# Kernel optimization log

Hardware: AMD Instinct MI355X
Metric: run time of the kernel (lower is better)

The kernel has to match this reference:

```python
import jax, jax.numpy as jnp
import numpy as np


def _banded_diag_mean(a, b, r):
    """For each (batch i, row j) return mean of (a[i] @ b[i].T)[j, j-r:j+r+1],
    computed without materializing the LxL matrix. Windows are clipped to
    [max(0,j-r), min(L, j+r+1)].  a, b: [B, L, D]."""
    B, L, _ = a.shape
    sums = jnp.zeros((B, L), a.dtype)
    counts = jnp.zeros((L,), a.dtype)
    for d in range(-r, r + 1):  # small fixed set of 2r+1 diagonals
        if d >= 0:
            dots = jnp.einsum('bld,bld->bl', a[:, :L - d], b[:, d:])
            sums = sums.at[:, :L - d].add(dots)
            counts = counts.at[:L - d].add(1.0)
        else:
            dots = jnp.einsum('bld,bld->bl', a[:, -d:], b[:, :L + d])
            sums = sums.at[:, -d:].add(dots)
            counts = counts.at[-d:].add(1.0)
    return sums / counts


def setup_inputs() -> dict:
    key = jax.random.key(0)
    k1, k2, k3 = jax.random.split(key, 3)
    B, L, D_in, D_feat = 8, 1024, 512, 256
    return {
        'feature1': jax.random.normal(k1, (B, L, D_in), jnp.float32),
        'feature2': jax.random.normal(k2, (B, L, D_in), jnp.float32),
        'W': jax.random.normal(k3, (D_in, D_feat), jnp.float32) / np.sqrt(D_in),
        'b': jnp.zeros((D_feat,), jnp.float32),
        'positive_range_self': 4,
        'positive_range_tgt': 4,
    }


def reference(feature1, feature2, W, b, positive_range_self, positive_range_tgt):
    # MLPLayer projection (shared eval_func for both inputs): linear + relu
    emb_1 = jax.nn.relu(feature1 @ W + b)  # [B, L, Df]
    emb_2 = jax.nn.relu(feature2 @ W + b)  # [B, L, Df]
    B, L, Df = emb_1.shape
    N = B * L

    positive = jnp.einsum('bld,bld->bl', emb_1, emb_2)  # [B, L]
    if positive_range_self > 0:
        positive = positive + _banded_diag_mean(emb_1, emb_1, positive_range_self)
        positive = positive + _banded_diag_mean(emb_2, emb_2, positive_range_self)
    if positive_range_tgt > 0:
        positive = positive + _banded_diag_mean(emb_1, emb_2, positive_range_tgt)
    positive = positive.reshape(N)

    e1 = emb_1.reshape(N, Df)
    e2 = emb_2.reshape(N, Df)
    sim_matrix = e1 @ e2.T  # [N, N]
    negative = jax.nn.logsumexp(sim_matrix, axis=-1) - jnp.log(jnp.asarray(N, sim_matrix.dtype))

    nce_loss = jnp.mean(-positive + negative)
    return nce_loss
```

## Files before the change

### kernel.cpp

```cpp
#include <hip/hip_runtime.h>
#include <hip/hip_bf16.h>
#include <math.h>

#define DIN 512
#define DF 256
#define LSEQ 1024
#define NTOT 8192

typedef __attribute__((ext_vector_type(8))) short short8;
typedef __attribute__((ext_vector_type(4))) short short4v;
typedef __attribute__((ext_vector_type(4))) float f32x4;

__device__ __forceinline__ short f2bf(float x) {
  union { float f; unsigned u; } un; un.f = x;
  unsigned r = un.u + 0x7fffu + ((un.u >> 16) & 1u);
  return (short)(r >> 16);
}
__device__ __forceinline__ float bf2f(short s) {
  union { unsigned u; float f; } un; un.u = ((unsigned)(unsigned short)s) << 16;
  return un.f;
}

typedef __attribute__((address_space(1))) const unsigned char AS1c;
typedef __attribute__((address_space(3))) unsigned char AS3;
__device__ __forceinline__ void gload16(const void* g, void* l) {
  __builtin_amdgcn_global_load_lds((AS1c*)g, (AS3*)l, 16, 0, 0);
}
#define CFENCE() asm volatile("" ::: "memory")

__global__ __launch_bounds__(256) void prep_w_kernel(const float* __restrict__ W,
                                                     short* __restrict__ Wt) {
  int idx = blockIdx.x * 256 + threadIdx.x;
  int c = idx >> 9;
  int k = idx & (DIN - 1);
  Wt[idx] = f2bf(W[(size_t)k * DF + c]);
}

#define PBM 64
#define PBK 64
#define PROW 72

__global__ __launch_bounds__(256) void proj_kernel(const float* __restrict__ f1,
                                                   const float* __restrict__ f2,
                                                   const short* __restrict__ Wt,
                                                   const float* __restrict__ bias,
                                                   short* __restrict__ emb1,
                                                   short* __restrict__ emb2) {
  const float* feat = blockIdx.y ? f2 : f1;
  short* emb = blockIdx.y ? emb2 : emb1;
  __shared__ short ldsA[PBM * PROW];
  __shared__ short ldsB[DF * PROW];
  const int tid = threadIdx.x;
  const int lane = tid & 63, wv = tid >> 6;
  const int wrow = (wv & 1) * 32, wcol = (wv >> 1) * 128;
  const int l15 = lane & 15, lk = (lane >> 4) * 8;
  const int rowbase = blockIdx.x * PBM;

  f32x4 acc[2][8];
#pragma unroll
  for (int mi = 0; mi < 2; ++mi)
#pragma unroll
    for (int nf = 0; nf < 8; ++nf) acc[mi][nf] = f32x4{0.f, 0.f, 0.f, 0.f};

  for (int kb = 0; kb < DIN; kb += PBK) {
    __syncthreads();
#pragma unroll
    for (int i = 0; i < 4; ++i) {
      int flat = tid * 4 + i;
      int r = flat >> 4, kq = (flat & 15) * 4;
      f32x4 v = *(const f32x4*)(feat + (size_t)(rowbase + r) * DIN + kb + kq);
      short4v h;
      h[0] = f2bf(v[0]); h[1] = f2bf(v[1]); h[2] = f2bf(v[2]); h[3] = f2bf(v[3]);
      *(short4v*)(ldsA + r * PROW + kq) = h;
    }
#pragma unroll
    for (int i = 0; i < 8; ++i) {
      int c = tid, kq = i * 8;
      short8 v = *(const short8*)(Wt + (size_t)c * DIN + kb + kq);
      *(short8*)(ldsB + c * PROW + kq) = v;
    }
    __syncthreads();
#pragma unroll
    for (int kk = 0; kk < 2; ++kk) {
      short8 af[2], bf[8];
#pragma unroll
      for (int mi = 0; mi < 2; ++mi)
        af[mi] = *(const short8*)(ldsA + (wrow + mi * 16 + l15) * PROW + kk * 32 + lk);
#pragma unroll
      for (int nf = 0; nf < 8; ++nf)
        bf[nf] = *(const short8*)(ldsB + (wcol + nf * 16 + l15) * PROW + kk * 32 + lk);
#pragma unroll
      for (int mi = 0; mi < 2; ++mi)
#pragma unroll
        for (int nf = 0; nf < 8; ++nf)
          acc[mi][nf] = __builtin_amdgcn_mfma_f32_16x16x32_bf16(af[mi], bf[nf], acc[mi][nf], 0, 0, 0);
    }
  }
  const int r4 = (lane >> 4) * 4;
#pragma unroll
  for (int mi = 0; mi < 2; ++mi) {
    int row0 = rowbase + wrow + mi * 16 + r4;
#pragma unroll
    for (int nf = 0; nf < 8; ++nf) {
      int col = wcol + nf * 16 + l15;
      float bb = bias[col];
#pragma unroll
      for (int r = 0; r < 4; ++r) {
        float v = acc[mi][nf][r] + bb;
        v = v > 0.f ? v : 0.f;
        emb[(size_t)(row0 + r) * DF + col] = f2bf(v);
      }
    }
  }
}

__global__ __launch_bounds__(64) void positive_kernel(const short* __restrict__ emb1,
                                                      const short* __restrict__ emb2,
                                                      const int* __restrict__ prs,
                                                      const int* __restrict__ prt,
                                                      float* __restrict__ pos) {
  const int row = blockIdx.x;
  const int b = row >> 10, j = row & (LSEQ - 1);
  const int lane = threadIdx.x;
  const int rs = prs[0], rt = prt[0];
  float a1[4], a2[4];
  {
    short4v v1 = *(const short4v*)(emb1 + (size_t)row * DF + lane * 4);
    short4v v2 = *(const short4v*)(emb2 + (size_t)row * DF + lane * 4);
#pragma unroll
    for (int i = 0; i < 4; ++i) { a1[i] = bf2f(v1[i]); a2[i] = bf2f(v2[i]); }
  }
  float dot12 = 0.f, p11 = 0.f, p22 = 0.f, p12 = 0.f;
#pragma unroll
  for (int i = 0; i < 4; ++i) dot12 += a1[i] * a2[i];
  int rmax = rs > rt ? rs : rt;
  for (int d = -rmax; d <= rmax; ++d) {
    int k = j + d;
    if (k < 0 || k >= LSEQ) continue;
    size_t koff = (size_t)(b * LSEQ + k) * DF + lane * 4;
    short4v w1 = *(const short4v*)(emb1 + koff);
    short4v w2 = *(const short4v*)(emb2 + koff);
    float d11 = 0.f, d22 = 0.f, d12 = 0.f;
#pragma unroll
    for (int i = 0; i < 4; ++i) {
      float e1k = bf2f(w1[i]), e2k = bf2f(w2[i]);
      d11 += a1[i] * e1k;
      d22 += a2[i] * e2k;
      d12 += a1[i] * e2k;
    }
    if (d >= -rs && d <= rs) { p11 += d11; p22 += d22; }
    if (d >= -rt && d <= rt) { p12 += d12; }
  }
#pragma unroll
  for (int m = 1; m < 64; m <<= 1) {
    dot12 += __shfl_xor(dot12, m);
    p11 += __shfl_xor(p11, m);
    p22 += __shfl_xor(p22, m);
    p12 += __shfl_xor(p12, m);
  }
  if (lane == 0) {
    float res = dot12;
    if (rs > 0) {
      int lo = j - rs < 0 ? 0 : j - rs;
      int hi = j + rs > LSEQ - 1 ? LSEQ - 1 : j + rs;
      res += (p11 + p22) / (float)(hi - lo + 1);
    }
    if (rt > 0) {
      int lo = j - rt < 0 ? 0 : j - rt;
      int hi = j + rt > LSEQ - 1 ? LSEQ - 1 : j + rt;
      res += p12 / (float)(hi - lo + 1);
    }
    pos[row] = res;
  }
}

#define NBM 128
#define NBN 32
#define NCHUNK 16
#define CHW (NTOT / NCHUNK)
#define NT (CHW / NBN)

__global__ __launch_bounds__(256, 3) void negative_kernel(const short* __restrict__ e1,
                                                          const short* __restrict__ e2,
                                                          float* __restrict__ mpart,
                                                          float* __restrict__ spart) {
  __shared__ short ldsB[2][NBN * DF];
  const int tid = threadIdx.x;
  const int lane = tid & 63, wv = tid >> 6;
  const int l15 = lane & 15, lk16 = lane >> 4;
  const int rowbase = blockIdx.x * NBM + wv * 32;
  const short* colbase = e2 + (size_t)(blockIdx.y * CHW) * DF;

  const int src_off = (tid & 31) * DF + (tid >> 5) * 8;
  const int dst_off = wv * 512;

  auto stage = [&](int tt) {
    const short* nb = colbase + (size_t)tt * NBN * DF + src_off;
    short* db = (short*)ldsB[tt & 1] + dst_off;
#pragma unroll
    for (int i = 0; i < 4; ++i)
      gload16(nb + i * 64, db + i * 2048);
  };

  stage(0);
  CFENCE();
  short8 a[2][8];
#pragma unroll
  for (int mi = 0; mi < 2; ++mi)
#pragma unroll
    for (int ks = 0; ks < 8; ++ks)
      a[mi][ks] = *(const short8*)(e1 + (size_t)(rowbase + mi * 16 + l15) * DF + ks * 32 + lk16 * 8);
  CFENCE();
  stage(1);
  CFENCE();

  float mrun[8], srun[8];
#pragma unroll
  for (int i = 0; i < 8; ++i) { mrun[i] = -1e30f; srun[i] = 0.f; }

  for (int t = 0; t < NT; ++t) {
    if (t < NT - 1) asm volatile("s_waitcnt vmcnt(4)" ::: "memory");
    else            asm volatile("s_waitcnt vmcnt(0)" ::: "memory");
    __builtin_amdgcn_s_barrier();
    const short* bbase = (const short*)ldsB[t & 1] + lk16 * 256 + l15 * 8;

    f32x4 acc[2][2];
#pragma unroll
    for (int mi = 0; mi < 2; ++mi)
#pragma unroll
      for (int nf = 0; nf < 2; ++nf) acc[mi][nf] = f32x4{0.f, 0.f, 0.f, 0.f};

    __builtin_amdgcn_s_setprio(1);
#pragma unroll
    for (int ks = 0; ks < 8; ++ks) {
      short8 b0 = *(const short8*)(bbase + ks * 1024);
      short8 b1 = *(const short8*)(bbase + ks * 1024 + 128);
#pragma unroll
      for (int mi = 0; mi < 2; ++mi) {
        acc[mi][0] = __builtin_amdgcn_mfma_f32_16x16x32_bf16(a[mi][ks], b0, acc[mi][0], 0, 0, 0);
        acc[mi][1] = __builtin_amdgcn_mfma_f32_16x16x32_bf16(a[mi][ks], b1, acc[mi][1], 0, 0, 0);
      }
    }
    __builtin_amdgcn_s_setprio(0);

#pragma unroll
    for (int mi = 0; mi < 2; ++mi)
#pragma unroll
      for (int r = 0; r < 4; ++r) {
        int s8 = mi * 4 + r;
        float v0 = acc[mi][0][r], v1 = acc[mi][1][r];
        float mo = mrun[s8];
        float mn = fmaxf(mo, fmaxf(v0, v1));
        mrun[s8] = mn;
        srun[s8] = srun[s8] * __expf(mo - mn) + __expf(v0 - mn) + __expf(v1 - mn);
      }
    __builtin_amdgcn_s_barrier();
    CFENCE();
    if (t + 2 < NT) stage(t + 2);
  }

#pragma unroll
  for (int mi = 0; mi < 2; ++mi)
#pragma unroll
    for (int r = 0; r < 4; ++r) {
      int s8 = mi * 4 + r;
      float m = mrun[s8], s = srun[s8];
#pragma unroll
      for (int msk = 1; msk < 16; msk <<= 1) {
        float mo = __shfl_xor(m, msk);
        float so = __shfl_xor(s, msk);
        float mn = fmaxf(m, mo);
        s = s * __expf(m - mn) + so * __expf(mo - mn);
        m = mn;
      }
      if (l15 == 0) {
        int row = rowbase + mi * 16 + lk16 * 4 + r;
        mpart[blockIdx.y * NTOT + row] = m;
        spart[blockIdx.y * NTOT + row] = s;
      }
    }
}

__global__ __launch_bounds__(256) void finalize1_kernel(const float* __restrict__ pos,
                                                        const float* __restrict__ mpart,
                                                        const float* __restrict__ spart,
                                                        float* __restrict__ partial) {
  __shared__ float red[4];
  int row = blockIdx.x * 256 + threadIdx.x;
  float m = -1e30f;
#pragma unroll
  for (int c = 0; c < NCHUNK; ++c) m = fmaxf(m, mpart[c * NTOT + row]);
  float s = 0.f;
#pragma unroll
  for (int c = 0; c < NCHUNK; ++c) s += spart[c * NTOT + row] * __expf(mpart[c * NTOT + row] - m);
  float v = m + logf(s) - pos[row];
#pragma unroll
  for (int msk = 1; msk < 64; msk <<= 1) v += __shfl_xor(v, msk);
  if ((threadIdx.x & 63) == 0) red[threadIdx.x >> 6] = v;
  __syncthreads();
  if (threadIdx.x == 0) partial[blockIdx.x] = red[0] + red[1] + red[2] + red[3];
}

__global__ __launch_bounds__(64) void finalize2_kernel(const float* __restrict__ partial,
                                                       float* __restrict__ out) {
  int lane = threadIdx.x;
  float v = lane < 32 ? partial[lane] : 0.f;
#pragma unroll
  for (int msk = 1; msk < 64; msk <<= 1) v += __shfl_xor(v, msk);
  if (lane == 0) out[0] = v / (float)NTOT - logf((float)NTOT);
}

extern "C" void kernel_launch(void* const* d_in, const int* in_sizes, int n_in,
                              void* d_out, int out_size, void* d_ws, size_t ws_size,
                              hipStream_t stream) {
  const float* f1 = (const float*)d_in[0];
  const float* f2 = (const float*)d_in[1];
  const float* W = (const float*)d_in[2];
  const float* bias = (const float*)d_in[3];
  const int* prs = (const int*)d_in[4];
  const int* prt = (const int*)d_in[5];
  float* out = (float*)d_out;

  char* ws = (char*)d_ws;
  short* Wt = (short*)(ws);
  short* emb1 = (short*)(ws + 262144);
  short* emb2 = (short*)(ws + 262144 + 4194304);
  float* pos = (float*)(ws + 8650752);
  float* mpart = (float*)(ws + 8683520);
  float* spart = (float*)(ws + 9207808);
  float* partial = (float*)(ws + 9732096);

  prep_w_kernel<<<(DF * DIN) / 256, 256, 0, stream>>>(W, Wt);
  proj_kernel<<<dim3(NTOT / PBM, 2), 256, 0, stream>>>(f1, f2, Wt, bias, emb1, emb2);
  positive_kernel<<<NTOT, 64, 0, stream>>>(emb1, emb2, prs, prt, pos);
  negative_kernel<<<dim3(NTOT / NBM, NCHUNK), 256, 0, stream>>>(emb1, emb2, mpart, spart);
  finalize1_kernel<<<32, 256, 0, stream>>>(pos, mpart, spart, partial);
  finalize2_kernel<<<1, 64, 0, stream>>>(partial, out);
}
```

Measured before the change: 93.96 us.

## Software-pipeline MFMA tiles with softmax and add lazy max rescaling

Restructures the logsumexp loop so that the MFMA products for tile t are computed while the online softmax for tile t-1 runs, using two ping-pong accumulator sets. It also adds a lazy-rescale path: the running max is updated only when a new value exceeds it by more than a threshold across the wave. Otherwise the exponentials are taken with exp2 against a precomputed scaled max. This aims to hide exp/VALU latency behind matrix work and cut the number of exponentials per tile. The costs are more accumulator registers and a wave-wide vote, and the sum can grow larger before rescaling.

```diff
diff --git a/kernel.cpp b/kernel.cpp
--- a/kernel.cpp
+++ b/kernel.cpp
@@ -27,6 +27,7 @@
   __builtin_amdgcn_global_load_lds((AS1c*)g, (AS3*)l, 16, 0, 0);
 }
 #define CFENCE() asm volatile("" ::: "memory")
+#define L2E 1.44269504089f
 
 __global__ __launch_bounds__(256) void prep_w_kernel(const float* __restrict__ W,
                                                      short* __restrict__ Wt) {
@@ -214,50 +215,83 @@
   stage(1);
   CFENCE();
 
-  float mrun[8], srun[8];
-#pragma unroll
-  for (int i = 0; i < 8; ++i) { mrun[i] = -1e30f; srun[i] = 0.f; }
-
-  for (int t = 0; t < NT; ++t) {
-    if (t < NT - 1) asm volatile("s_waitcnt vmcnt(4)" ::: "memory");
-    else            asm volatile("s_waitcnt vmcnt(0)" ::: "memory");
-    __builtin_amdgcn_s_barrier();
-    const short* bbase = (const short*)ldsB[t & 1] + lk16 * 256 + l15 * 8;
-
-    f32x4 acc[2][2];
-#pragma unroll
-    for (int mi = 0; mi < 2; ++mi)
-#pragma unroll
-      for (int nf = 0; nf < 2; ++nf) acc[mi][nf] = f32x4{0.f, 0.f, 0.f, 0.f};
-
-    __builtin_amdgcn_s_setprio(1);
-#pragma unroll
-    for (int ks = 0; ks < 8; ++ks) {
-      short8 b0 = *(const short8*)(bbase + ks * 1024);
-      short8 b1 = *(const short8*)(bbase + ks * 1024 + 128);
-#pragma unroll
-      for (int mi = 0; mi < 2; ++mi) {
-        acc[mi][0] = __builtin_amdgcn_mfma_f32_16x16x32_bf16(a[mi][ks], b0, acc[mi][0], 0, 0, 0);
-        acc[mi][1] = __builtin_amdgcn_mfma_f32_16x16x32_bf16(a[mi][ks], b1, acc[mi][1], 0, 0, 0);
-      }
-    }
-    __builtin_amdgcn_s_setprio(0);
-
-#pragma unroll
-    for (int mi = 0; mi < 2; ++mi)
-#pragma unroll
-      for (int r = 0; r < 4; ++r) {
-        int s8 = mi * 4 + r;
-        float v0 = acc[mi][0][r], v1 = acc[mi][1][r];
-        float mo = mrun[s8];
-        float mn = fmaxf(mo, fmaxf(v0, v1));
-        mrun[s8] = mn;
-        srun[s8] = srun[s8] * __expf(mo - mn) + __expf(v0 - mn) + __expf(v1 - mn);
-      }
-    __builtin_amdgcn_s_barrier();
-    CFENCE();
-    if (t + 2 < NT) stage(t + 2);
-  }
+  float mrun[8], srun[8], moL[8];
+#pragma unroll
+  for (int i = 0; i < 8; ++i) { mrun[i] = -1e30f; srun[i] = 0.f; moL[i] = -1e30f; }
+
+  f32x4 pA[2][2], pB[2][2];
+
+#define COMPUTE(P, t)                                                          \
+  {                                                                            \
+    if ((t) < NT - 1) asm volatile("s_waitcnt vmcnt(4)" ::: "memory");         \
+    else              asm volatile("s_waitcnt vmcnt(0)" ::: "memory");         \
+    __builtin_amdgcn_s_barrier();                                              \
+    const short* bbase = (const short*)ldsB[(t) & 1] + lk16 * 256 + l15 * 8;   \
+    _Pragma("unroll")                                                          \
+    for (int ks = 0; ks < 8; ++ks) {                                           \
+      short8 b0 = *(const short8*)(bbase + ks * 1024);                         \
+      short8 b1 = *(const short8*)(bbase + ks * 1024 + 128);                   \
+      if (ks == 0) {                                                           \
+        P[0][0] = __builtin_amdgcn_mfma_f32_16x16x32_bf16(a[0][0], b0, f32x4{0.f,0.f,0.f,0.f}, 0, 0, 0); \
+        P[0][1] = __builtin_amdgcn_mfma_f32_16x16x32_bf16(a[0][0], b1, f32x4{0.f,0.f,0.f,0.f}, 0, 0, 0); \
+        P[1][0] = __builtin_amdgcn_mfma_f32_16x16x32_bf16(a[1][0], b0, f32x4{0.f,0.f,0.f,0.f}, 0, 0, 0); \
+        P[1][1] = __builtin_amdgcn_mfma_f32_16x16x32_bf16(a[1][0], b1, f32x4{0.f,0.f,0.f,0.f}, 0, 0, 0); \
+      } else {                                                                 \
+        P[0][0] = __builtin_amdgcn_mfma_f32_16x16x32_bf16(a[0][ks], b0, P[0][0], 0, 0, 0); \
+        P[0][1] = __builtin_amdgcn_mfma_f32_16x16x32_bf16(a[0][ks], b1, P[0][1], 0, 0, 0); \
+        P[1][0] = __builtin_amdgcn_mfma_f32_16x16x32_bf16(a[1][ks], b0, P[1][0], 0, 0, 0); \
+        P[1][1] = __builtin_amdgcn_mfma_f32_16x16x32_bf16(a[1][ks], b1, P[1][1], 0, 0, 0); \
+      }                                                                        \
+    }                                                                          \
+  }
+
+#define SOFTMAX(Q)                                                             \
+  {                                                                            \
+    float mx[8];                                                               \
+    bool nd = false;                                                           \
+    _Pragma("unroll")                                                          \
+    for (int s = 0; s < 8; ++s) {                                              \
+      mx[s] = fmaxf(Q[s >> 2][0][s & 3], Q[s >> 2][1][s & 3]);                 \
+      nd = nd || (mx[s] > mrun[s] + 8.f);                                      \
+    }                                                                          \
+    if (__any(nd)) {                                                           \
+      _Pragma("unroll")                                                        \
+      for (int s = 0; s < 8; ++s) {                                            \
+        float mo = mrun[s];                                                    \
+        float mn = fmaxf(mo, mx[s]);                                           \
+        mrun[s] = mn; moL[s] = mn * L2E;                                       \
+        srun[s] = srun[s] * __expf(mo - mn)                                    \
+                + __expf(Q[s >> 2][0][s & 3] - mn)                             \
+                + __expf(Q[s >> 2][1][s & 3] - mn);                            \
+      }                                                                        \
+    } else {                                                                   \
+      _Pragma("unroll")                                                        \
+      for (int s = 0; s < 8; ++s) {                                            \
+        srun[s] += exp2f(__builtin_fmaf(Q[s >> 2][0][s & 3], L2E, -moL[s]))    \
+                 + exp2f(__builtin_fmaf(Q[s >> 2][1][s & 3], L2E, -moL[s]));   \
+      }                                                                        \
+    }                                                                          \
+  }
+
+#define TILE(P, Q, t)                                                          \
+  {                                                                            \
+    COMPUTE(P, t);                                                             \
+    SOFTMAX(Q);                                                                \
+    __builtin_amdgcn_s_barrier();                                              \
+    CFENCE();                                                                  \
+    if ((t) + 2 < NT) stage((t) + 2);                                          \
+  }
+
+  COMPUTE(pA, 0);
+  __builtin_amdgcn_s_barrier();
+  CFENCE();
+  stage(2);
+  for (int tp = 0; tp < 7; ++tp) {
+    TILE(pB, pA, 2 * tp + 1);
+    TILE(pA, pB, 2 * tp + 2);
+  }
+  TILE(pB, pA, 15);
+  SOFTMAX(pB);
 
 #pragma unroll
   for (int mi = 0; mi < 2; ++mi)
@@ -279,6 +313,9 @@
         spart[blockIdx.y * NTOT + row] = s;
       }
     }
+#undef COMPUTE
+#undef SOFTMAX
+#undef TILE
 }
 
 __global__ __launch_bounds__(256) void finalize1_kernel(const float* __restrict__ pos,
```

Measured after the change: 100.3 us. 1.07x slower.

## Use lazy base-2 online logsumexp with threshold rescale and smaller column tile

Applied to the files above, without the earlier changes.

The negative-logsumexp kernel now keeps its running max in log2 units and works with exp2. It only rescales the running sum when some lane's scaled logit exceeds the current max by a threshold (wave-wide __any check), and otherwise just adds exp2 of the difference. The column tile shrinks from 32 to 16, with occupancy bumped to 4 blocks per SM, to cut per-wave exponential work and register pressure. The aim is to cut transcendental and max/rescale overhead in the online softmax. The risk is more barriers and iterations per tile, plus possible float overflow if growth between rescales stays under the threshold for many steps.

```diff
diff --git a/kernel.cpp b/kernel.cpp
--- a/kernel.cpp
+++ b/kernel.cpp
@@ -27,6 +27,9 @@
   __builtin_amdgcn_global_load_lds((AS1c*)g, (AS3*)l, 16, 0, 0);
 }
 #define CFENCE() asm volatile("" ::: "memory")
+#define L2E 1.44269504089f
+#define THRL 11.5416f
+#define LN2 0.69314718056f
 
 __global__ __launch_bounds__(256) void prep_w_kernel(const float* __restrict__ W,
                                                      short* __restrict__ Wt) {
@@ -175,12 +178,12 @@
 }
 
 #define NBM 128
-#define NBN 32
+#define NBN 16
 #define NCHUNK 16
 #define CHW (NTOT / NCHUNK)
 #define NT (CHW / NBN)
 
-__global__ __launch_bounds__(256, 3) void negative_kernel(const short* __restrict__ e1,
+__global__ __launch_bounds__(256, 4) void negative_kernel(const short* __restrict__ e1,
                                                           const short* __restrict__ e2,
                                                           float* __restrict__ mpart,
                                                           float* __restrict__ spart) {
@@ -191,15 +194,15 @@
   const int rowbase = blockIdx.x * NBM + wv * 32;
   const short* colbase = e2 + (size_t)(blockIdx.y * CHW) * DF;
 
-  const int src_off = (tid & 31) * DF + (tid >> 5) * 8;
+  const int src_off = (tid & 15) * DF + (tid >> 4) * 8;
   const int dst_off = wv * 512;
 
   auto stage = [&](int tt) {
     const short* nb = colbase + (size_t)tt * NBN * DF + src_off;
     short* db = (short*)ldsB[tt & 1] + dst_off;
 #pragma unroll
-    for (int i = 0; i < 4; ++i)
-      gload16(nb + i * 64, db + i * 2048);
+    for (int i = 0; i < 2; ++i)
+      gload16(nb + i * 128, db + i * 2048);
   };
 
   stage(0);
@@ -214,71 +217,70 @@
   stage(1);
   CFENCE();
 
-  float mrun[8], srun[8];
-#pragma unroll
-  for (int i = 0; i < 8; ++i) { mrun[i] = -1e30f; srun[i] = 0.f; }
+  float mrunL[8], srun[8];
+#pragma unroll
+  for (int i = 0; i < 8; ++i) { mrunL[i] = 0.f; srun[i] = 0.f; }
 
   for (int t = 0; t < NT; ++t) {
-    if (t < NT - 1) asm volatile("s_waitcnt vmcnt(4)" ::: "memory");
+    if (t < NT - 1) asm volatile("s_waitcnt vmcnt(2)" ::: "memory");
     else            asm volatile("s_waitcnt vmcnt(0)" ::: "memory");
     __builtin_amdgcn_s_barrier();
-    const short* bbase = (const short*)ldsB[t & 1] + lk16 * 256 + l15 * 8;
-
-    f32x4 acc[2][2];
-#pragma unroll
-    for (int mi = 0; mi < 2; ++mi)
-#pragma unroll
-      for (int nf = 0; nf < 2; ++nf) acc[mi][nf] = f32x4{0.f, 0.f, 0.f, 0.f};
-
+    const short* bbase = (const short*)ldsB[t & 1] + lk16 * 128 + l15 * 8;
+
+    f32x4 acc0 = f32x4{0.f, 0.f, 0.f, 0.f};
+    f32x4 acc1 = f32x4{0.f, 0.f, 0.f, 0.f};
     __builtin_amdgcn_s_setprio(1);
 #pragma unroll
     for (int ks = 0; ks < 8; ++ks) {
-      short8 b0 = *(const short8*)(bbase + ks * 1024);
-      short8 b1 = *(const short8*)(bbase + ks * 1024 + 128);
-#pragma unroll
-      for (int mi = 0; mi < 2; ++mi) {
-        acc[mi][0] = __builtin_amdgcn_mfma_f32_16x16x32_bf16(a[mi][ks], b0, acc[mi][0], 0, 0, 0);
-        acc[mi][1] = __builtin_amdgcn_mfma_f32_16x16x32_bf16(a[mi][ks], b1, acc[mi][1], 0, 0, 0);
-      }
+      short8 b0 = *(const short8*)(bbase + ks * 512);
+      acc0 = __builtin_amdgcn_mfma_f32_16x16x32_bf16(a[0][ks], b0, acc0, 0, 0, 0);
+      acc1 = __builtin_amdgcn_mfma_f32_16x16x32_bf16(a[1][ks], b0, acc1, 0, 0, 0);
     }
     __builtin_amdgcn_s_setprio(0);
-
-#pragma unroll
-    for (int mi = 0; mi < 2; ++mi)
-#pragma unroll
-      for (int r = 0; r < 4; ++r) {
-        int s8 = mi * 4 + r;
-        float v0 = acc[mi][0][r], v1 = acc[mi][1][r];
-        float mo = mrun[s8];
-        float mn = fmaxf(mo, fmaxf(v0, v1));
-        mrun[s8] = mn;
-        srun[s8] = srun[s8] * __expf(mo - mn) + __expf(v0 - mn) + __expf(v1 - mn);
-      }
     __builtin_amdgcn_s_barrier();
     CFENCE();
     if (t + 2 < NT) stage(t + 2);
-  }
-
-#pragma unroll
-  for (int mi = 0; mi < 2; ++mi)
-#pragma unroll
-    for (int r = 0; r < 4; ++r) {
-      int s8 = mi * 4 + r;
-      float m = mrun[s8], s = srun[s8];
-#pragma unroll
-      for (int msk = 1; msk < 16; msk <<= 1) {
-        float mo = __shfl_xor(m, msk);
-        float so = __shfl_xor(s, msk);
-        float mn = fmaxf(m, mo);
-        s = s * __expf(m - mn) + so * __expf(mo - mn);
-        m = mn;
+
+    float args[8];
+    bool nd = false;
+#pragma unroll
+    for (int s = 0; s < 8; ++s) {
+      float v = (s < 4) ? acc0[s] : acc1[s - 4];
+      args[s] = __builtin_fmaf(v, L2E, -mrunL[s]);
+      nd = nd || (args[s] > THRL);
+    }
+    if (__any(nd)) {
+#pragma unroll
+      for (int s = 0; s < 8; ++s) {
+        float vL = args[s] + mrunL[s];
+        float mnL = fmaxf(mrunL[s], vL);
+        srun[s] = srun[s] * exp2f(mrunL[s] - mnL) + exp2f(vL - mnL);
+        mrunL[s] = mnL;
       }
-      if (l15 == 0) {
-        int row = rowbase + mi * 16 + lk16 * 4 + r;
-        mpart[blockIdx.y * NTOT + row] = m;
-        spart[blockIdx.y * NTOT + row] = s;
-      }
-    }
+    } else {
+#pragma unroll
+      for (int s = 0; s < 8; ++s)
+        srun[s] += exp2f(args[s]);
+    }
+  }
+
+#pragma unroll
+  for (int s = 0; s < 8; ++s) {
+    float m = mrunL[s], sv = srun[s];
+#pragma unroll
+    for (int msk = 1; msk < 16; msk <<= 1) {
+      float mo = __shfl_xor(m, msk);
+      float so = __shfl_xor(sv, msk);
+      float mn = fmaxf(m, mo);
+      sv = sv * exp2f(m - mn) + so * exp2f(mo - mn);
+      m = mn;
+    }
+    if (l15 == 0) {
+      int row = rowbase + (s >> 2) * 16 + lk16 * 4 + (s & 3);
+      mpart[blockIdx.y * NTOT + row] = m;
+      spart[blockIdx.y * NTOT + row] = sv;
+    }
+  }
 }
 
 __global__ __launch_bounds__(256) void finalize1_kernel(const float* __restrict__ pos,
@@ -292,8 +294,8 @@
   for (int c = 0; c < NCHUNK; ++c) m = fmaxf(m, mpart[c * NTOT + row]);
   float s = 0.f;
 #pragma unroll
-  for (int c = 0; c < NCHUNK; ++c) s += spart[c * NTOT + row] * __expf(mpart[c * NTOT + row] - m);
-  float v = m + logf(s) - pos[row];
+  for (int c = 0; c < NCHUNK; ++c) s += spart[c * NTOT + row] * exp2f(mpart[c * NTOT + row] - m);
+  float v = (m + log2f(s)) * LN2 - pos[row];
 #pragma unroll
   for (int msk = 1; msk < 64; msk <<= 1) v += __shfl_xor(v, msk);
   if ((threadIdx.x & 63) == 0) red[threadIdx.x >> 6] = v;
```

Result: slower. 123.9 us (+31.9%).
